# Kernel optimization log

Hardware: AMD Instinct MI355X
Metric: run time of the kernel (lower is better)

The kernel has to match this reference:

```python
import jax, jax.numpy as jnp
import numpy as np

N = 8192

def setup_inputs() -> dict:
    key = jax.random.key(0)
    k1, k2 = jax.random.split(key)
    estimated_adj = jax.random.uniform(k1, (N, N), dtype=jnp.float32)
    ori = jax.random.uniform(k2, (N, N), dtype=jnp.float32)
    return {"estimated_adj": estimated_adj, "ori": ori}

def reference(estimated_adj, ori):
    # normalize(): adj = estimated_adj * ori; mx = adj + I; row-normalize.
    n = estimated_adj.shape[0]
    mx = estimated_adj * ori + jnp.eye(n, dtype=estimated_adj.dtype)
    rowsum = mx.sum(axis=1)  # [n]
    r_inv = jnp.power(rowsum, -1.0)
    r_inv = jnp.where(jnp.isinf(r_inv), 0.0, r_inv)
    # diag(r_inv) @ mx is mathematically a per-row scale; do it without the O(n^3) GEMM.
    return r_inv[:, None] * mx
```

## Files before the change

kernel.cpp:

```cpp
#include <hip/hip_runtime.h>
#include <math.h>


#define NDIM 8192
#define BLOCK 1024
#define WAVES (BLOCK / 64)
#define V4_PER_THREAD (NDIM / 4 / BLOCK)
#define ROW_BYTES (NDIM * 4)
#define CHUNK_BYTES 1024
#define CHUNKS (ROW_BYTES / CHUNK_BYTES)
#define CHUNKS_PER_WAVE (CHUNKS / WAVES)

typedef float f32x4 __attribute__((ext_vector_type(4)));
typedef __attribute__((address_space(3))) unsigned int lds_u32;
typedef const __attribute__((address_space(1))) unsigned int glb_u32;

__device__ __forceinline__ void dma16(const void* g, void* lds) {
    __builtin_amdgcn_global_load_lds((glb_u32*)g, (lds_u32*)lds, 16, 0, 0);
}

__global__ __launch_bounds__(BLOCK, 8) void row_normalize_kernel(
    const float* __restrict__ a,
    const float* __restrict__ b,
    float* __restrict__ out)
{
    __shared__ f32x4 bufA[NDIM / 4];
    __shared__ f32x4 bufB[NDIM / 4];
    __shared__ double wave_sums[WAVES];

    const int row  = blockIdx.x;
    const int tid  = threadIdx.x;
    const int lane = tid & 63;
    const int wave = tid >> 6;

    const char* arow = (const char*)(a + (size_t)row * NDIM);
    const char* brow = (const char*)(b + (size_t)row * NDIM);
    f32x4* __restrict__ o4 = (f32x4*)(out + (size_t)row * NDIM);

#pragma unroll
    for (int k = 0; k < CHUNKS_PER_WAVE; ++k) {
        const int c = wave * CHUNKS_PER_WAVE + k;
        const int goff = c * CHUNK_BYTES + lane * 16;
        dma16(arow + goff, (char*)bufA + c * CHUNK_BYTES);
        dma16(brow + goff, (char*)bufB + c * CHUNK_BYTES);
    }
    asm volatile("s_waitcnt vmcnt(0)" ::: "memory");
    __syncthreads();

    double sum = 0.0;
#pragma unroll
    for (int i = 0; i < V4_PER_THREAD; ++i) {
        const int idx = tid + i * BLOCK;
        f32x4 p = bufA[idx] * bufB[idx];
        const int col0 = idx << 2;
        if ((unsigned)(row - col0) < 4u) {
            if      (row == col0)     p.x += 1.0f;
            else if (row == col0 + 1) p.y += 1.0f;
            else if (row == col0 + 2) p.z += 1.0f;
            else                      p.w += 1.0f;
        }
        bufA[idx] = p;
        sum += (double)p.x + (double)p.y + (double)p.z + (double)p.w;
    }

#pragma unroll
    for (int off = 32; off > 0; off >>= 1)
        sum += __shfl_down(sum, off, 64);

    if (lane == 0) wave_sums[wave] = sum;
    __syncthreads();

    double total = 0.0;
#pragma unroll
    for (int w = 0; w < WAVES; ++w) total += wave_sums[w];
    float r_inv = 1.0f / (float)total;
    if (isinf(r_inv)) r_inv = 0.0f;

#pragma unroll
    for (int i = 0; i < V4_PER_THREAD; ++i) {
        const int idx = tid + i * BLOCK;
        f32x4 p = bufA[idx];
        p *= r_inv;
        o4[idx] = p;
    }
}

extern "C" void kernel_launch(void* const* d_in, const int* in_sizes, int n_in,
                              void* d_out, int out_size, void* d_ws, size_t ws_size,
                              hipStream_t stream) {
    const float* a = (const float*)d_in[0];
    const float* b = (const float*)d_in[1];
    float* out = (float*)d_out;
    row_normalize_kernel<<<NDIM, BLOCK, 0, stream>>>(a, b, out);
}
```

Measured before the change: 580.4 us.

## Use persistent blocks with double-buffered LDS DMA prefetch across rows

```diff
diff --git a/kernel.cpp b/kernel.cpp
--- a/kernel.cpp
+++ b/kernel.cpp
@@ -5,11 +5,14 @@
 #define NDIM 8192
 #define BLOCK 1024
 #define WAVES (BLOCK / 64)
-#define V4_PER_THREAD (NDIM / 4 / BLOCK)
+#define GRID 256
+#define RPB (NDIM / GRID)
 #define ROW_BYTES (NDIM * 4)
+#define F4_PER_THREAD (NDIM / 4 / BLOCK)
 #define CHUNK_BYTES 1024
-#define CHUNKS (ROW_BYTES / CHUNK_BYTES)
-#define CHUNKS_PER_WAVE (CHUNKS / WAVES)
+#define CHUNKS_PER_MAT (ROW_BYTES / CHUNK_BYTES)
+#define CPW (CHUNKS_PER_MAT / WAVES)
+#define SMEM_BYTES (4 * 32768)
 
 typedef float f32x4 __attribute__((ext_vector_type(4)));
 typedef __attribute__((address_space(3))) unsigned int lds_u32;
@@ -19,69 +22,92 @@
     __builtin_amdgcn_global_load_lds((glb_u32*)g, (lds_u32*)lds, 16, 0, 0);
 }
 
-__global__ __launch_bounds__(BLOCK, 8) void row_normalize_kernel(
+__global__ __launch_bounds__(BLOCK) void row_normalize_kernel(
     const float* __restrict__ a,
     const float* __restrict__ b,
     float* __restrict__ out)
 {
-    __shared__ f32x4 bufA[NDIM / 4];
-    __shared__ f32x4 bufB[NDIM / 4];
+    extern __shared__ char smem[];
     __shared__ double wave_sums[WAVES];
 
-    const int row  = blockIdx.x;
     const int tid  = threadIdx.x;
     const int lane = tid & 63;
     const int wave = tid >> 6;
+    const int bid  = blockIdx.x;
 
-    const char* arow = (const char*)(a + (size_t)row * NDIM);
-    const char* brow = (const char*)(b + (size_t)row * NDIM);
-    f32x4* __restrict__ o4 = (f32x4*)(out + (size_t)row * NDIM);
+
+    auto dmaMat = [&](const float* src, int k, char* dst) {
+        const size_t row = (size_t)(bid + k * GRID);
+        const char* g = (const char*)src + row * (size_t)ROW_BYTES;
+#pragma unroll
+        for (int j = 0; j < CPW; ++j) {
+            const int off = (wave * CPW + j) * CHUNK_BYTES;
+            dma16(g + off + lane * 16, dst + off);
+        }
+    };
+
+    dmaMat(a, 0, smem);                 dmaMat(b, 0, smem + 65536);
+    dmaMat(a, 1, smem + 32768);         dmaMat(b, 1, smem + 98304);
+
+    for (int k = 0; k < RPB; ++k) {
+        const int par = k & 1;
+        const int row = bid + k * GRID;
+        char* const pa = smem + par * 32768;
+        char* const pb = smem + 65536 + par * 32768;
+
+        if (k == 0)            asm volatile("s_waitcnt vmcnt(4)\ns_barrier" ::: "memory");
+        else if (k == RPB - 1) asm volatile("s_waitcnt vmcnt(0)\ns_barrier" ::: "memory");
+        else                   asm volatile("s_waitcnt vmcnt(6)\ns_barrier" ::: "memory");
+        __builtin_amdgcn_sched_barrier(0);
+
+        const f32x4* A4 = (const f32x4*)pa;
+        const f32x4* B4 = (const f32x4*)pb;
+        f32x4*       P4 = (f32x4*)pa;
+
+        double sum = 0.0;
+#pragma unroll
+        for (int i = 0; i < F4_PER_THREAD; ++i) {
+            const int idx = tid + i * BLOCK;
+            f32x4 p = A4[idx] * B4[idx];
+            const int col0 = idx << 2;
+            if ((unsigned)(row - col0) < 4u) {
+                if      (row == col0)     p.x += 1.0f;
+                else if (row == col0 + 1) p.y += 1.0f;
+                else if (row == col0 + 2) p.z += 1.0f;
+                else                      p.w += 1.0f;
+            }
+            P4[idx] = p;
+            sum += (double)p.x + (double)p.y + (double)p.z + (double)p.w;
+        }
 
 #pragma unroll
-    for (int k = 0; k < CHUNKS_PER_WAVE; ++k) {
-        const int c = wave * CHUNKS_PER_WAVE + k;
-        const int goff = c * CHUNK_BYTES + lane * 16;
-        dma16(arow + goff, (char*)bufA + c * CHUNK_BYTES);
-        dma16(brow + goff, (char*)bufB + c * CHUNK_BYTES);
-    }
-    asm volatile("s_waitcnt vmcnt(0)" ::: "memory");
-    __syncthreads();
+        for (int off = 32; off > 0; off >>= 1)
+            sum += __shfl_down(sum, off, 64);
+        if (lane == 0) wave_sums[wave] = sum;
 
-    double sum = 0.0;
+        asm volatile("s_waitcnt lgkmcnt(0)\ns_barrier" ::: "memory");
+        __builtin_amdgcn_sched_barrier(0);
+
+        if (k + 2 < RPB) dmaMat(b, k + 2, pb);
+
+        double total = 0.0;
 #pragma unroll
-    for (int i = 0; i < V4_PER_THREAD; ++i) {
-        const int idx = tid + i * BLOCK;
-        f32x4 p = bufA[idx] * bufB[idx];
-        const int col0 = idx << 2;
-        if ((unsigned)(row - col0) < 4u) {
-            if      (row == col0)     p.x += 1.0f;
-            else if (row == col0 + 1) p.y += 1.0f;
-            else if (row == col0 + 2) p.z += 1.0f;
-            else                      p.w += 1.0f;
+        for (int w = 0; w < WAVES; ++w) total += wave_sums[w];
+        float r_inv = 1.0f / (float)total;
+        if (isinf(r_inv)) r_inv = 0.0f;
+
+        f32x4* __restrict__ o4 = (f32x4*)(out + (size_t)row * NDIM);
+#pragma unroll
+        for (int i = 0; i < F4_PER_THREAD; ++i) {
+            const int idx = tid + i * BLOCK;
+            f32x4 p = P4[idx];
+            p *= r_inv;
+            o4[idx] = p;
         }
-        bufA[idx] = p;
-        sum += (double)p.x + (double)p.y + (double)p.z + (double)p.w;
-    }
 
-#pragma unroll
-    for (int off = 32; off > 0; off >>= 1)
-        sum += __shfl_down(sum, off, 64);
-
-    if (lane == 0) wave_sums[wave] = sum;
-    __syncthreads();
-
-    double total = 0.0;
-#pragma unroll
-    for (int w = 0; w < WAVES; ++w) total += wave_sums[w];
-    float r_inv = 1.0f / (float)total;
-    if (isinf(r_inv)) r_inv = 0.0f;
-
-#pragma unroll
-    for (int i = 0; i < V4_PER_THREAD; ++i) {
-        const int idx = tid + i * BLOCK;
-        f32x4 p = bufA[idx];
-        p *= r_inv;
-        o4[idx] = p;
+        asm volatile("s_barrier" ::: "memory");
+        __builtin_amdgcn_sched_barrier(0);
+        if (k + 2 < RPB) dmaMat(a, k + 2, pa);
     }
 }
 
@@ -91,5 +117,12 @@
     const float* a = (const float*)d_in[0];
     const float* b = (const float*)d_in[1];
     float* out = (float*)d_out;
-    row_normalize_kernel<<<NDIM, BLOCK, 0, stream>>>(a, b, out);
+
+    static bool init = false;
+    if (!init) {
+        (void)hipFuncSetAttribute((const void*)row_normalize_kernel,
+                                  hipFuncAttributeMaxDynamicSharedMemorySize, SMEM_BYTES);
+        init = true;
+    }
+    row_normalize_kernel<<<GRID, BLOCK, SMEM_BYTES, stream>>>(a, b, out);
 }
```

Result: no change. 586.9 us (+1.1%).
